# Performance work log

Hardware: AMD Instinct MI355X
Metric: run time of the kernel (lower is better)

The kernel has to match this reference:

```python
import jax, jax.numpy as jnp
from jax import lax
import numpy as np

B, C, T = 4096, 22, 1001   # batch, EEG channels, time samples
K, KSZ, P = 40, 25, 100    # num_kernels, kernel_size, pool_size
S, O = 9, 4                # num_subjects, n_outputs
FEAT = K * ((T - KSZ + 1) // P)  # 40*9 = 360
BN_EPS = 1e-5


def setup_inputs() -> dict:
    key = jax.random.key(0)
    ks = jax.random.split(key, 8)
    x = jax.random.normal(ks[0], (B, C, T + 1), dtype=jnp.float32)
    # subject ids in 1..S encoded as id*1e6 in the last time step (all channels; only ch 0 is read)
    ids = jax.random.randint(ks[1], (B,), 1, S + 1)
    x = x.at[:, :, -1].set((ids * 1000000).astype(jnp.float32)[:, None])
    conv_w = jax.random.normal(ks[2], (K, C, 1, KSZ), dtype=jnp.float32) * 0.05
    conv_b = jax.random.normal(ks[3], (K,), dtype=jnp.float32) * 0.05
    bn_gamma = jnp.ones((K,), dtype=jnp.float32)
    bn_beta = jnp.zeros((K,), dtype=jnp.float32)
    fc_w = jax.random.normal(ks[4], (S, FEAT, O), dtype=jnp.float32) * 0.05
    fc_b = jax.random.normal(ks[5], (S, O), dtype=jnp.float32) * 0.05
    return {"x": x, "conv_w": conv_w, "conv_b": conv_b,
            "bn_gamma": bn_gamma, "bn_beta": bn_beta,
            "fc_w": fc_w, "fc_b": fc_b}


def reference(x, conv_w, conv_b, bn_gamma, bn_beta, fc_w, fc_b):
    # subject index (0-based); int cast blocks gradient flow, matching .item() dispatch
    sid = jnp.round(x[:, 0, -1] / 1e6).astype(jnp.int32) - 1  # [B]
    xin = x[:, :, :-1][:, :, None, :]                          # [B, C, 1, T]
    # Conv2d(n_chans, num_kernels, (1, kernel_size)), VALID padding
    y = lax.conv_general_dilated(xin, conv_w, window_strides=(1, 1),
                                 padding='VALID',
                                 dimension_numbers=('NCHW', 'OIHW', 'NCHW'))
    y = y + conv_b[None, :, None, None]                        # [B, K, 1, W], W = T-KSZ+1
    y = jax.nn.elu(y)
    # BatchNorm2d with batch statistics (train mode), affine
    mean = jnp.mean(y, axis=(0, 2, 3), keepdims=True)
    var = jnp.var(y, axis=(0, 2, 3), keepdims=True)
    y = (y - mean) * lax.rsqrt(var + BN_EPS)
    y = y * bn_gamma[None, :, None, None] + bn_beta[None, :, None, None]
    # AvgPool2d((1, P)): non-overlapping windows, remainder dropped
    W = y.shape[-1]
    n = W // P
    y = y[:, :, 0, :n * P].reshape(B, K, n, P).mean(axis=-1)   # [B, K, n]
    feat = y.reshape(B, -1)                                     # [B, FEAT]
    # dropout is identity at inference
    # per-sample subject-indexed FC, vectorized as a gathered batched matvec
    out = jnp.einsum('bf,bfo->bo', feat, fc_w[sid]) + fc_b[sid]  # [B, O]
    return out
```

## Files before the change

### kernel.cpp

```cpp
#include <hip/hip_runtime.h>

#define BATCH 4096
#define CCH   22
#define TT    1001
#define TROW  1002
#define KOUT  40
#define KSZ   25
#define WOUT  977
#define POOLW 100
#define NWIN  9
#define FEAT  360
#define NOUT  4

#define WBLK  512
#define NWB   2
#define NBLK  (BATCH * NWB)
#define CSTG  24
#define ROWB  48
#define TSTG  544
#define FKK   19
#define KP    48
#define NLOC  7
#define NMT   8

typedef __attribute__((ext_vector_type(8))) short short8;
typedef __attribute__((ext_vector_type(4))) float floatx4;

__device__ __forceinline__ unsigned short f2bf(float f) {
    unsigned u = __float_as_uint(f);
    u += 0x7fff + ((u >> 16) & 1);
    return (unsigned short)(u >> 16);
}
__device__ __forceinline__ unsigned cvt_pk_bf16(float a, float b) {
    unsigned r;
    asm("v_cvt_pk_bf16_f32 %0, %1, %2" : "=v"(r) : "v"(a), "v"(b));
    return r;
}
__device__ __forceinline__ float eluf(float v) {
    return v > 0.0f ? v : __expf(v) - 1.0f;
}

__global__ __launch_bounds__(256) void pack_w_kernel(const float* __restrict__ cw,
                                                     unsigned short* __restrict__ wp) {
    int i = blockIdx.x * 256 + threadIdx.x;
    if (i >= FKK * KP * 32) return;
    int e = i & 31;
    int n = (i >> 5) % KP;
    int kk = i / (KP * 32);
    int f = kk * 32 + e;
    int j = f / CSTG, c = f - j * CSTG;
    float v = (n < KOUT && c < CCH && j < KSZ) ? cw[(n * CCH + c) * KSZ + j] : 0.0f;
    wp[i] = f2bf(v);
}

__global__ __launch_bounds__(256, 3) void conv_mfma_kernel(
        const float* __restrict__ x, const unsigned short* __restrict__ wp,
        const float* __restrict__ cb, float* __restrict__ pparts,
        float* __restrict__ spS, float* __restrict__ spQ) {
    __shared__ unsigned short xt[TSTG * CSTG];
    __shared__ float ps_s[NLOC * KP];
    __shared__ float st_q[KP];

    const int bx = blockIdx.x, b = blockIdx.y;
    const int w0     = bx ? 488 : 0;
    const int ostart = bx ? 500 : 0;
    const int oend   = bx ? WOUT : 500;
    const int win0   = bx ? 4 : 0;
    const int tid = threadIdx.x;
    const int wv = __builtin_amdgcn_readfirstlane(tid >> 6);
    const int lane = tid & 63;
    const size_t xb = (size_t)b * (CCH * TROW);

    for (int i = tid; i < NLOC * KP + KP; i += 256) {
        if (i < NLOC * KP) ps_s[i] = 0.0f;
        else st_q[i - NLOC * KP] = 0.0f;
    }

    {
        const int r5 = lane & 31, h = lane >> 5;
#pragma unroll
        for (int it = 0; it < 5; ++it) {
            int idx = it * 4 + wv;
            if (idx < 17) {
                int t_loc = idx * 32 + r5;
                int t_gl = w0 + t_loc;
                float v[12];
#pragma unroll
                for (int r = 0; r < 12; ++r) {
                    int c = h * 12 + r;
                    v[r] = (c < CCH && t_gl < TT) ? x[xb + (size_t)c * TROW + t_gl] : 0.0f;
                }
                unsigned u[6];
#pragma unroll
                for (int r = 0; r < 6; ++r) u[r] = cvt_pk_bf16(v[2 * r], v[2 * r + 1]);
                char* dst = (char*)xt + t_loc * ROWB + h * 24;
                *(uint2*)(dst)      = make_uint2(u[0], u[1]);
                *(uint2*)(dst + 8)  = make_uint2(u[2], u[3]);
                *(uint2*)(dst + 16) = make_uint2(u[4], u[5]);
            }
        }
    }
    __syncthreads();

    const int m16 = lane & 15, g = lane >> 4;
    floatx4 acc[NMT][3];
#pragma unroll
    for (int nt = 0; nt < 3; ++nt) {
        int k = nt * 16 + m16;
        float bv = (k < KOUT) ? cb[k] : 0.0f;
#pragma unroll
        for (int mt = 0; mt < NMT; ++mt) acc[mt][nt] = (floatx4){bv, bv, bv, bv};
    }

    const char* ap = (const char*)xt + (wv * 128 + m16) * ROWB + g * 16;
    const unsigned short* wpl = wp + m16 * 32 + g * 8;

    short8 bfr[3];
#pragma unroll
    for (int nt = 0; nt < 3; ++nt)
        bfr[nt] = *(const short8*)(wpl + nt * 16 * 32);

#pragma unroll 1
    for (int kk = 0; kk < FKK; ++kk) {
        short8 bnx[3];
        if (kk + 1 < FKK) {
            const unsigned short* wn = wpl + (kk + 1) * (KP * 32);
#pragma unroll
            for (int nt = 0; nt < 3; ++nt)
                bnx[nt] = *(const short8*)(wn + nt * 16 * 32);
        }
#pragma unroll
        for (int half = 0; half < 2; ++half) {
            short8 afr[4];
#pragma unroll
            for (int q = 0; q < 4; ++q)
                afr[q] = *(const short8*)(ap + (half * 4 + q) * (16 * ROWB));
#pragma unroll
            for (int q = 0; q < 4; ++q)
#pragma unroll
                for (int nt = 0; nt < 3; ++nt)
                    acc[half * 4 + q][nt] = __builtin_amdgcn_mfma_f32_16x16x32_bf16(
                        afr[q], bfr[nt], acc[half * 4 + q][nt], 0, 0, 0);
        }
        ap += 64;
#pragma unroll
        for (int nt = 0; nt < 3; ++nt) bfr[nt] = bnx[nt];
    }

    float qv[3] = {0.f, 0.f, 0.f};
#pragma unroll
    for (int mt = 0; mt < NMT; ++mt) {
        const int wbase = w0 + wv * 128 + mt * 16 + g * 4;
        const int win = wbase / POOLW;
#pragma unroll
        for (int nt = 0; nt < 3; ++nt) {
            const int k = nt * 16 + m16;
            const bool kok = (k < KOUT);
            float psum = 0.f;
#pragma unroll
            for (int r = 0; r < 4; ++r) {
                int w = wbase + r;
                float e = eluf(acc[mt][nt][r]);
                e = (kok && w >= ostart && w < oend) ? e : 0.0f;
                psum += e;
                qv[nt] = fmaf(e, e, qv[nt]);
            }
            float o1 = __shfl_down(psum, 16); int w1 = __shfl_down(win, 16);
            if (lane < 48 && w1 == win) psum += o1;
            float o2 = __shfl_down(psum, 32); int w2 = __shfl_down(win, 32);
            if (lane < 32 && w2 == win) psum += o2;
            int wu = __shfl_up(win, 16);
            if (g == 0 || wu != win)
                atomicAdd(&ps_s[(win - win0) * KP + k], psum);
        }
    }
#pragma unroll
    for (int nt = 0; nt < 3; ++nt) {
        float q = qv[nt];
        q += __shfl_xor(q, 16);
        q += __shfl_xor(q, 32);
        if (g == 0) atomicAdd(&st_q[nt * 16 + m16], q);
    }
    __syncthreads();

    const int blk = b * NWB + bx;
    if (tid < KOUT) {
        float s = 0.0f;
#pragma unroll
        for (int wl = 0; wl < NLOC; ++wl) s += ps_s[wl * KP + tid];
        spS[(size_t)tid * NBLK + blk] = s;
        spQ[(size_t)tid * NBLK + blk] = st_q[tid];
    }
    for (int i = tid; i < NLOC * KOUT; i += 256) {
        int wl = i / KOUT, k = i - wl * KOUT;
        pparts[((size_t)blk * NLOC + wl) * KOUT + k] = ps_s[wl * KP + k];
    }
}

__global__ __launch_bounds__(256) void bn_stats_kernel(
        const float* __restrict__ spS, const float* __restrict__ spQ,
        const float* __restrict__ gamma, const float* __restrict__ beta,
        float* __restrict__ scale, float* __restrict__ shift) {
    const int k = blockIdx.x;
    float s = 0.0f, q = 0.0f;
    for (int r = threadIdx.x; r < NBLK; r += 256) {
        s += spS[(size_t)k * NBLK + r];
        q += spQ[(size_t)k * NBLK + r];
    }
#pragma unroll
    for (int m = 32; m; m >>= 1) {
        s += __shfl_xor(s, m, 64);
        q += __shfl_xor(q, m, 64);
    }
    __shared__ float rs[4], rq[4];
    const int wid = threadIdx.x >> 6, lane = threadIdx.x & 63;
    if (lane == 0) { rs[wid] = s; rq[wid] = q; }
    __syncthreads();
    if (threadIdx.x == 0) {
        s = rs[0] + rs[1] + rs[2] + rs[3];
        q = rq[0] + rq[1] + rq[2] + rq[3];
        const float N = (float)BATCH * (float)WOUT;
        float mean = s / N;
        float var = q / N - mean * mean;
        float sc = gamma[k] / sqrtf(var + 1e-5f);
        scale[k] = sc;
        shift[k] = beta[k] - mean * sc;
    }
}

__global__ __launch_bounds__(64) void fc_kernel(
        const float* __restrict__ x, const float* __restrict__ pparts,
        const float* __restrict__ scale, const float* __restrict__ shift,
        const float* __restrict__ fcw, const float* __restrict__ fcb,
        float* __restrict__ out) {
    const int b = blockIdx.x;
    const int lane = threadIdx.x;
    const float idv = x[(size_t)b * (CCH * TROW) + TT];
    const int sid = (int)(idv * 1e-6f + 0.5f) - 1;
    const float* W = fcw + (size_t)sid * (FEAT * NOUT);
    const float* base = pparts + (size_t)b * (NWB * NLOC * KOUT);
    float a0 = 0, a1 = 0, a2 = 0, a3 = 0;
    for (int f = lane; f < FEAT; f += 64) {
        int k = f / NWIN, win = f - k * NWIN;
        int u = (win < 5) ? win : (win + 3);
        float p = base[u * KOUT + k];
        float feat = fmaf(p * 0.01f, scale[k], shift[k]);
        a0 = fmaf(feat, W[f * 4 + 0], a0);
        a1 = fmaf(feat, W[f * 4 + 1], a1);
        a2 = fmaf(feat, W[f * 4 + 2], a2);
        a3 = fmaf(feat, W[f * 4 + 3], a3);
    }
#pragma unroll
    for (int m = 32; m; m >>= 1) {
        a0 += __shfl_xor(a0, m, 64);
        a1 += __shfl_xor(a1, m, 64);
        a2 += __shfl_xor(a2, m, 64);
        a3 += __shfl_xor(a3, m, 64);
    }
    if (lane == 0) {
        out[b * 4 + 0] = a0 + fcb[sid * 4 + 0];
        out[b * 4 + 1] = a1 + fcb[sid * 4 + 1];
        out[b * 4 + 2] = a2 + fcb[sid * 4 + 2];
        out[b * 4 + 3] = a3 + fcb[sid * 4 + 3];
    }
}

extern "C" void kernel_launch(void* const* d_in, const int* in_sizes, int n_in,
                              void* d_out, int out_size, void* d_ws, size_t ws_size,
                              hipStream_t stream) {
    const float* x     = (const float*)d_in[0];
    const float* cw    = (const float*)d_in[1];
    const float* cb    = (const float*)d_in[2];
    const float* gamma = (const float*)d_in[3];
    const float* beta  = (const float*)d_in[4];
    const float* fcw   = (const float*)d_in[5];
    const float* fcb   = (const float*)d_in[6];
    float* out = (float*)d_out;

    float* pparts = (float*)d_ws;
    float* spS    = pparts + (size_t)NBLK * NLOC * KOUT;
    float* spQ    = spS + (size_t)KOUT * NBLK;
    float* scale  = spQ + (size_t)KOUT * NBLK;
    float* shift  = scale + KOUT;
    unsigned short* wpck = (unsigned short*)(shift + KOUT);

    pack_w_kernel<<<(FKK * KP * 32 + 255) / 256, 256, 0, stream>>>(cw, wpck);
    conv_mfma_kernel<<<dim3(NWB, BATCH), 256, 0, stream>>>(x, wpck, cb, pparts, spS, spQ);
    bn_stats_kernel<<<KOUT, 256, 0, stream>>>(spS, spQ, gamma, beta, scale, shift);
    fc_kernel<<<BATCH, 64, 0, stream>>>(x, pparts, scale, shift, fcw, fcb, out);
}
```

Before: 307.0 us.

## Make conv kernel persistent with double-buffered prefetch of next work unit

The conv kernel now has each block process 16 consecutive (batch, half-window) units in a loop instead of one unit per block. The global loads for the next unit are issued into registers before the MFMA loop, then converted and stored into a second shared-memory buffer afterwards, so load latency overlaps compute. This adds register pressure (60 extra floats per thread), doubles shared memory, lowers the occupancy hint from 3 to 2 blocks per CU, and shrinks the grid to 512 blocks, which may leave compute units underused.

```diff
diff --git a/kernel.cpp b/kernel.cpp
--- a/kernel.cpp
+++ b/kernel.cpp
@@ -12,9 +12,10 @@
 #define FEAT  360
 #define NOUT  4
 
-#define WBLK  512
 #define NWB   2
 #define NBLK  (BATCH * NWB)
+#define NU    16
+#define NGRID (NBLK / NU)
 #define CSTG  24
 #define ROWB  48
 #define TSTG  544
@@ -53,31 +54,32 @@
     wp[i] = f2bf(v);
 }
 
-__global__ __launch_bounds__(256, 3) void conv_mfma_kernel(
+__global__ __launch_bounds__(256, 2) void conv_mfma_kernel(
         const float* __restrict__ x, const unsigned short* __restrict__ wp,
         const float* __restrict__ cb, float* __restrict__ pparts,
         float* __restrict__ spS, float* __restrict__ spQ) {
-    __shared__ unsigned short xt[TSTG * CSTG];
-    __shared__ float ps_s[NLOC * KP];
-    __shared__ float st_q[KP];
-
-    const int bx = blockIdx.x, b = blockIdx.y;
-    const int w0     = bx ? 488 : 0;
-    const int ostart = bx ? 500 : 0;
-    const int oend   = bx ? WOUT : 500;
-    const int win0   = bx ? 4 : 0;
+    __shared__ unsigned short xt[2][TSTG * CSTG];
+    __shared__ float ps_s[2][NLOC * KP];
+    __shared__ float st_q[2][KP];
+
     const int tid = threadIdx.x;
     const int wv = __builtin_amdgcn_readfirstlane(tid >> 6);
     const int lane = tid & 63;
-    const size_t xb = (size_t)b * (CCH * TROW);
-
-    for (int i = tid; i < NLOC * KP + KP; i += 256) {
-        if (i < NLOC * KP) ps_s[i] = 0.0f;
-        else st_q[i - NLOC * KP] = 0.0f;
+    const int r5 = lane & 31, h = lane >> 5;
+    const int m16 = lane & 15, g = lane >> 4;
+    const int u0 = blockIdx.x * NU;
+
+    for (int i = tid; i < 2 * (NLOC * KP + KP); i += 256) {
+        int sel = (i >= NLOC * KP + KP) ? 1 : 0;
+        int j = i - sel * (NLOC * KP + KP);
+        if (j < NLOC * KP) ps_s[sel][j] = 0.0f;
+        else st_q[sel][j - NLOC * KP] = 0.0f;
     }
 
     {
-        const int r5 = lane & 31, h = lane >> 5;
+        const int b = u0 >> 1, bx = u0 & 1;
+        const int w0 = bx ? 488 : 0;
+        const size_t xb = (size_t)b * (CCH * TROW);
 #pragma unroll
         for (int it = 0; it < 5; ++it) {
             int idx = it * 4 + wv;
@@ -90,110 +92,163 @@
                     int c = h * 12 + r;
                     v[r] = (c < CCH && t_gl < TT) ? x[xb + (size_t)c * TROW + t_gl] : 0.0f;
                 }
-                unsigned u[6];
-#pragma unroll
-                for (int r = 0; r < 6; ++r) u[r] = cvt_pk_bf16(v[2 * r], v[2 * r + 1]);
-                char* dst = (char*)xt + t_loc * ROWB + h * 24;
-                *(uint2*)(dst)      = make_uint2(u[0], u[1]);
-                *(uint2*)(dst + 8)  = make_uint2(u[2], u[3]);
-                *(uint2*)(dst + 16) = make_uint2(u[4], u[5]);
+                unsigned uu[6];
+#pragma unroll
+                for (int r = 0; r < 6; ++r) uu[r] = cvt_pk_bf16(v[2 * r], v[2 * r + 1]);
+                char* dst = (char*)xt[0] + t_loc * ROWB + h * 24;
+                *(uint2*)(dst)      = make_uint2(uu[0], uu[1]);
+                *(uint2*)(dst + 8)  = make_uint2(uu[2], uu[3]);
+                *(uint2*)(dst + 16) = make_uint2(uu[4], uu[5]);
             }
         }
     }
     __syncthreads();
 
-    const int m16 = lane & 15, g = lane >> 4;
-    floatx4 acc[NMT][3];
-#pragma unroll
-    for (int nt = 0; nt < 3; ++nt) {
-        int k = nt * 16 + m16;
-        float bv = (k < KOUT) ? cb[k] : 0.0f;
-#pragma unroll
-        for (int mt = 0; mt < NMT; ++mt) acc[mt][nt] = (floatx4){bv, bv, bv, bv};
-    }
-
-    const char* ap = (const char*)xt + (wv * 128 + m16) * ROWB + g * 16;
-    const unsigned short* wpl = wp + m16 * 32 + g * 8;
-
-    short8 bfr[3];
-#pragma unroll
-    for (int nt = 0; nt < 3; ++nt)
-        bfr[nt] = *(const short8*)(wpl + nt * 16 * 32);
-
 #pragma unroll 1
-    for (int kk = 0; kk < FKK; ++kk) {
-        short8 bnx[3];
-        if (kk + 1 < FKK) {
-            const unsigned short* wn = wpl + (kk + 1) * (KP * 32);
-#pragma unroll
-            for (int nt = 0; nt < 3; ++nt)
-                bnx[nt] = *(const short8*)(wn + nt * 16 * 32);
-        }
-#pragma unroll
-        for (int half = 0; half < 2; ++half) {
-            short8 afr[4];
-#pragma unroll
-            for (int q = 0; q < 4; ++q)
-                afr[q] = *(const short8*)(ap + (half * 4 + q) * (16 * ROWB));
-#pragma unroll
-            for (int q = 0; q < 4; ++q)
-#pragma unroll
-                for (int nt = 0; nt < 3; ++nt)
-                    acc[half * 4 + q][nt] = __builtin_amdgcn_mfma_f32_16x16x32_bf16(
-                        afr[q], bfr[nt], acc[half * 4 + q][nt], 0, 0, 0);
-        }
-        ap += 64;
-#pragma unroll
-        for (int nt = 0; nt < 3; ++nt) bfr[nt] = bnx[nt];
-    }
-
-    float qv[3] = {0.f, 0.f, 0.f};
-#pragma unroll
-    for (int mt = 0; mt < NMT; ++mt) {
-        const int wbase = w0 + wv * 128 + mt * 16 + g * 4;
-        const int win = wbase / POOLW;
+    for (int i = 0; i < NU; ++i) {
+        const int u = u0 + i;
+        const int b = u >> 1, bx = u & 1;
+        const int w0     = bx ? 488 : 0;
+        const int ostart = bx ? 500 : 0;
+        const int oend   = bx ? WOUT : 500;
+        const int win0   = bx ? 4 : 0;
+        const int cur = i & 1, nxt = cur ^ 1;
+        const bool hn = (i + 1 < NU);
+        const int uN = u + 1;
+        const int bxN = uN & 1;
+        const int w0N = bxN ? 488 : 0;
+        const size_t xbN = (size_t)(uN >> 1) * (CCH * TROW);
+
+        float vs[5][12];
+        if (hn) {
+#pragma unroll
+            for (int it = 0; it < 5; ++it) {
+                int idx = it * 4 + wv;
+                if (idx < 17) {
+                    int t_loc = idx * 32 + r5;
+                    int t_gl = w0N + t_loc;
+#pragma unroll
+                    for (int r = 0; r < 12; ++r) {
+                        int c = h * 12 + r;
+                        vs[it][r] = (c < CCH && t_gl < TT)
+                                        ? x[xbN + (size_t)c * TROW + t_gl] : 0.0f;
+                    }
+                }
+            }
+        }
+
+        floatx4 acc[NMT][3];
 #pragma unroll
         for (int nt = 0; nt < 3; ++nt) {
-            const int k = nt * 16 + m16;
-            const bool kok = (k < KOUT);
-            float psum = 0.f;
-#pragma unroll
-            for (int r = 0; r < 4; ++r) {
-                int w = wbase + r;
-                float e = eluf(acc[mt][nt][r]);
-                e = (kok && w >= ostart && w < oend) ? e : 0.0f;
-                psum += e;
-                qv[nt] = fmaf(e, e, qv[nt]);
-            }
-            float o1 = __shfl_down(psum, 16); int w1 = __shfl_down(win, 16);
-            if (lane < 48 && w1 == win) psum += o1;
-            float o2 = __shfl_down(psum, 32); int w2 = __shfl_down(win, 32);
-            if (lane < 32 && w2 == win) psum += o2;
-            int wu = __shfl_up(win, 16);
-            if (g == 0 || wu != win)
-                atomicAdd(&ps_s[(win - win0) * KP + k], psum);
-        }
-    }
-#pragma unroll
-    for (int nt = 0; nt < 3; ++nt) {
-        float q = qv[nt];
-        q += __shfl_xor(q, 16);
-        q += __shfl_xor(q, 32);
-        if (g == 0) atomicAdd(&st_q[nt * 16 + m16], q);
-    }
-    __syncthreads();
-
-    const int blk = b * NWB + bx;
-    if (tid < KOUT) {
-        float s = 0.0f;
-#pragma unroll
-        for (int wl = 0; wl < NLOC; ++wl) s += ps_s[wl * KP + tid];
-        spS[(size_t)tid * NBLK + blk] = s;
-        spQ[(size_t)tid * NBLK + blk] = st_q[tid];
-    }
-    for (int i = tid; i < NLOC * KOUT; i += 256) {
-        int wl = i / KOUT, k = i - wl * KOUT;
-        pparts[((size_t)blk * NLOC + wl) * KOUT + k] = ps_s[wl * KP + k];
+            int k = nt * 16 + m16;
+            float bv = (k < KOUT) ? cb[k] : 0.0f;
+#pragma unroll
+            for (int mt = 0; mt < NMT; ++mt) acc[mt][nt] = (floatx4){bv, bv, bv, bv};
+        }
+        const char* ap = (const char*)xt[cur] + (wv * 128 + m16) * ROWB + g * 16;
+        const unsigned short* wq = wp + m16 * 32 + g * 8;
+
+        short8 bfr[3];
+#pragma unroll
+        for (int nt = 0; nt < 3; ++nt) bfr[nt] = *(const short8*)(wq + nt * 16 * 32);
+
+#pragma unroll 1
+        for (int kk = 0; kk < FKK; ++kk) {
+            short8 bnx[3];
+            if (kk + 1 < FKK) {
+                const unsigned short* wn = wq + (kk + 1) * (KP * 32);
+#pragma unroll
+                for (int nt = 0; nt < 3; ++nt) bnx[nt] = *(const short8*)(wn + nt * 16 * 32);
+            }
+#pragma unroll
+            for (int half = 0; half < 2; ++half) {
+                short8 afr[4];
+#pragma unroll
+                for (int q = 0; q < 4; ++q)
+                    afr[q] = *(const short8*)(ap + kk * 64 + (half * 4 + q) * (16 * ROWB));
+#pragma unroll
+                for (int q = 0; q < 4; ++q)
+#pragma unroll
+                    for (int nt = 0; nt < 3; ++nt)
+                        acc[half * 4 + q][nt] = __builtin_amdgcn_mfma_f32_16x16x32_bf16(
+                            afr[q], bfr[nt], acc[half * 4 + q][nt], 0, 0, 0);
+            }
+#pragma unroll
+            for (int nt = 0; nt < 3; ++nt) bfr[nt] = bnx[nt];
+        }
+
+        if (hn) {
+#pragma unroll
+            for (int it = 0; it < 5; ++it) {
+                int idx = it * 4 + wv;
+                if (idx < 17) {
+                    int t_loc = idx * 32 + r5;
+                    unsigned uu[6];
+#pragma unroll
+                    for (int r = 0; r < 6; ++r)
+                        uu[r] = cvt_pk_bf16(vs[it][2 * r], vs[it][2 * r + 1]);
+                    char* dst = (char*)xt[nxt] + t_loc * ROWB + h * 24;
+                    *(uint2*)(dst)      = make_uint2(uu[0], uu[1]);
+                    *(uint2*)(dst + 8)  = make_uint2(uu[2], uu[3]);
+                    *(uint2*)(dst + 16) = make_uint2(uu[4], uu[5]);
+                }
+            }
+        }
+
+        for (int z = tid; z < NLOC * KP + KP; z += 256) {
+            if (z < NLOC * KP) ps_s[nxt][z] = 0.0f;
+            else st_q[nxt][z - NLOC * KP] = 0.0f;
+        }
+
+        float qv[3] = {0.f, 0.f, 0.f};
+#pragma unroll
+        for (int mt = 0; mt < NMT; ++mt) {
+            const int wbase = w0 + wv * 128 + mt * 16 + g * 4;
+            const int win = wbase / POOLW;
+#pragma unroll
+            for (int nt = 0; nt < 3; ++nt) {
+                const int k = nt * 16 + m16;
+                const bool kok = (k < KOUT);
+                float psum = 0.f;
+#pragma unroll
+                for (int r = 0; r < 4; ++r) {
+                    int w = wbase + r;
+                    float e = eluf(acc[mt][nt][r]);
+                    e = (kok && w >= ostart && w < oend) ? e : 0.0f;
+                    psum += e;
+                    qv[nt] = fmaf(e, e, qv[nt]);
+                }
+                float o1 = __shfl_down(psum, 16); int w1 = __shfl_down(win, 16);
+                if (lane < 48 && w1 == win) psum += o1;
+                float o2 = __shfl_down(psum, 32); int w2 = __shfl_down(win, 32);
+                if (lane < 32 && w2 == win) psum += o2;
+                int wu = __shfl_up(win, 16);
+                if (g == 0 || wu != win)
+                    atomicAdd(&ps_s[cur][(win - win0) * KP + k], psum);
+            }
+        }
+#pragma unroll
+        for (int nt = 0; nt < 3; ++nt) {
+            float q = qv[nt];
+            q += __shfl_xor(q, 16);
+            q += __shfl_xor(q, 32);
+            if (g == 0) atomicAdd(&st_q[cur][nt * 16 + m16], q);
+        }
+        __syncthreads();
+
+        const int blk = u;
+        if (tid < KOUT) {
+            float s = 0.0f;
+#pragma unroll
+            for (int wl = 0; wl < NLOC; ++wl) s += ps_s[cur][wl * KP + tid];
+            spS[(size_t)tid * NBLK + blk] = s;
+            spQ[(size_t)tid * NBLK + blk] = st_q[cur][tid];
+        }
+        for (int z = tid; z < NLOC * KOUT; z += 256) {
+            int wl = z / KOUT, k = z - wl * KOUT;
+            pparts[((size_t)blk * NLOC + wl) * KOUT + k] = ps_s[cur][wl * KP + k];
+        }
+        __syncthreads();
     }
 }
 
@@ -285,7 +340,7 @@
     unsigned short* wpck = (unsigned short*)(shift + KOUT);
 
     pack_w_kernel<<<(FKK * KP * 32 + 255) / 256, 256, 0, stream>>>(cw, wpck);
-    conv_mfma_kernel<<<dim3(NWB, BATCH), 256, 0, stream>>>(x, wpck, cb, pparts, spS, spQ);
+    conv_mfma_kernel<<<NGRID, 256, 0, stream>>>(x, wpck, cb, pparts, spS, spQ);
     bn_stats_kernel<<<KOUT, 256, 0, stream>>>(spS, spQ, gamma, beta, scale, shift);
     fc_kernel<<<BATCH, 64, 0, stream>>>(x, pparts, scale, shift, fcw, fcb, out);
 }
```

Result: no change. 310.5 us (+1.1%).
